# Performance work log

Hardware: AMD Instinct MI355X
Metric: run time of the kernel (lower is better)

## Reference

```python
import jax, jax.numpy as jnp
import numpy as np

N = 50000      # total nodes (batched protein graphs)
D = 256        # prot_hidden_dim
E = 800000     # edges per relation type
R = 5          # edge types: SEQ, STR_KNN, STR_DIS, SURF, LRR_REGION
LN_EPS = 1e-5
SIGMOID_TEMP = 2.0
WEIGHT_SCALE = 2.0
MIN_W, MAX_W = 0.05, 2.0


def setup_inputs() -> dict:
    key = jax.random.key(0)
    ks = jax.random.split(key, 8)
    x = jax.random.normal(ks[0], (N, D), dtype=jnp.float32)
    src = jax.random.randint(ks[1], (R, E), 0, N)
    dst = jax.random.randint(ks[2], (R, E), 0, N)
    # relation-attention MLP params: Linear(D, D//4) -> LayerNorm(D//4) -> ReLU -> Linear(D//4, 1)
    H = D // 4
    W1 = jax.random.normal(ks[3], (D, H), dtype=jnp.float32) / np.float32(np.sqrt(D))
    b1 = jnp.zeros((H,), jnp.float32)
    gamma = jnp.ones((H,), jnp.float32)
    beta = jnp.zeros((H,), jnp.float32)
    W2 = jax.random.normal(ks[4], (H, 1), dtype=jnp.float32) / np.float32(np.sqrt(H))
    b2 = jnp.zeros((1,), jnp.float32)
    attn_bias = jnp.array([-4.0, -4.0, -4.0, -4.0, -2.772], jnp.float32)
    return {"x": x, "src": src, "dst": dst, "W1": W1, "b1": b1,
            "gamma": gamma, "beta": beta, "W2": W2, "b2": b2,
            "attn_bias": attn_bias}


def _mean_aggregate(x, s, d):
    # DGL update_all(copy_u('h','m'), mean('m','h')): scatter-mean of src feats onto dst.
    sums = jax.ops.segment_sum(x[s], d, num_segments=N)                      # [N, D]
    cnt = jax.ops.segment_sum(jnp.ones((E,), x.dtype), d, num_segments=N)    # [N]
    # zero in-degree nodes get 0 (DGL mean semantics)
    return jnp.where(cnt[:, None] > 0, sums / jnp.maximum(cnt, 1.0)[:, None], 0.0)


def reference(x, src, dst, W1, b1, gamma, beta, W2, b2, attn_bias):
    # per-relation mean aggregation (loop over fixed small R, not a data dim)
    agg = jnp.stack([_mean_aggregate(x, src[r], dst[r]) for r in range(R)])  # [R, N, D]
    g = agg.mean(axis=1)                                                     # [R, D]
    # relation-attention MLP (dropout = identity in eval)
    h = g @ W1 + b1                                                          # [R, D//4]
    mu = h.mean(axis=-1, keepdims=True)
    var = ((h - mu) ** 2).mean(axis=-1, keepdims=True)
    h = (h - mu) * jax.lax.rsqrt(var + LN_EPS) * gamma + beta
    h = jax.nn.relu(h)
    scores = (h @ W2 + b2)[:, 0] + attn_bias                                 # [R]
    w = jax.nn.sigmoid(scores / SIGMOID_TEMP) * WEIGHT_SCALE
    w = jnp.clip(w, MIN_W, MAX_W)
    # fused = sum_r w[r] * agg[r]
    return jnp.einsum('r,rnd->nd', w, agg)
```

## Files before the change

### kernel.cpp

```cpp
#include <hip/hip_runtime.h>

#define NN 50000
#define DD 256
#define EE 800000
#define RR 5
#define HH 64
#define RN (RR * NN)

#define F_OFF  (RN)
#define F_CUR  (2 * RN)
#define F_C    (3 * RN)
#define F_G    (4 * RN)
#define F_W    (4 * RN + 1280)
#define F_CTR  (4 * RN + 1288)
#define F_ESRC (4 * RN + 1296)
#define F_XH   (F_ESRC + RR * EE)
#define BYTES_BF16 ((size_t)(F_XH + NN * DD / 2) * 4)
#define BYTES_F32  ((size_t)(F_ESRC + RR * EE) * 4)

#define C2_OFF  (RN)
#define C2_CUR  (2 * RN)
#define C2_G    (3 * RN)
#define C2_W    (3 * RN + 1280)
#define C2_CTR  (3 * RN + 1288)
#define C2_ESRC (3 * RN + 1296)
#define BYTES_CSR2 ((size_t)(C2_ESRC + RR * EE) * 4)

__device__ inline unsigned short bf16rn(float f) {
    unsigned u = __float_as_uint(f);
    unsigned r = u + 0x7FFFu + ((u >> 16) & 1u);
    return (unsigned short)(r >> 16);
}

__global__ __launch_bounds__(256) void deg_kernel(const int* __restrict__ dst,
                                                  int* __restrict__ cnt) {
    int i = blockIdx.x * 256 + threadIdx.x;
    if (i < RR * EE) {
        int r = i / EE;
        atomicAdd(&cnt[r * NN + dst[i]], 1);
    }
}

__global__ __launch_bounds__(256) void off_kernel(int* cnt, int* __restrict__ off,
                                                  int* __restrict__ cur,
                                                  int* __restrict__ ctr, float* invc) {
    int i = blockIdx.x * 256 + threadIdx.x;
    if (i < RN) {
        int cv = cnt[i];
        int o = atomicAdd(ctr, cv);
        off[i] = o;
        cur[i] = o;
        invc[i] = (cv > 0) ? (1.0f / (float)cv) : 0.0f;
    }
}

template <bool WITH_C>
__global__ __launch_bounds__(256) void fill_kernel(const int* __restrict__ src,
                                                   const int* __restrict__ dst,
                                                   int* __restrict__ cur,
                                                   int* __restrict__ esrc,
                                                   const float* __restrict__ invc,
                                                   float* __restrict__ c) {
    int i = blockIdx.x * 256 + threadIdx.x;
    if (i < RR * EE) {
        int r = i / EE;
        int d = dst[i];
        int s = src[i];
        int slot = atomicAdd(&cur[r * NN + d], 1);
        esrc[slot] = s;
        if constexpr (WITH_C) {
            unsafeAtomicAdd(&c[r * NN + s], invc[r * NN + d]);
        }
    }
}

__global__ __launch_bounds__(256) void gmat_kernel(const float* __restrict__ x,
                                                   const float* __restrict__ c,
                                                   float* __restrict__ g) {
    const int wave = threadIdx.x >> 6;
    const int lane = threadIdx.x & 63;
    const int gw = blockIdx.x * 4 + wave;
    const int nw = gridDim.x * 4;
    float4 a0 = {0, 0, 0, 0}, a1 = {0, 0, 0, 0}, a2 = {0, 0, 0, 0},
           a3 = {0, 0, 0, 0}, a4 = {0, 0, 0, 0};
    for (int s = gw; s < NN; s += nw) {
        float4 v = ((const float4*)(x + (size_t)s * DD))[lane];
        float c0 = c[0 * NN + s], c1 = c[1 * NN + s], c2 = c[2 * NN + s],
              c3 = c[3 * NN + s], c4 = c[4 * NN + s];
        a0.x += c0 * v.x; a0.y += c0 * v.y; a0.z += c0 * v.z; a0.w += c0 * v.w;
        a1.x += c1 * v.x; a1.y += c1 * v.y; a1.z += c1 * v.z; a1.w += c1 * v.w;
        a2.x += c2 * v.x; a2.y += c2 * v.y; a2.z += c2 * v.z; a2.w += c2 * v.w;
        a3.x += c3 * v.x; a3.y += c3 * v.y; a3.z += c3 * v.z; a3.w += c3 * v.w;
        a4.x += c4 * v.x; a4.y += c4 * v.y; a4.z += c4 * v.z; a4.w += c4 * v.w;
    }
    float4 acc[5] = {a0, a1, a2, a3, a4};
    #pragma unroll
    for (int r = 0; r < RR; ++r) {
        float* gr = g + r * DD + lane * 4;
        unsafeAtomicAdd(gr + 0, acc[r].x);
        unsafeAtomicAdd(gr + 1, acc[r].y);
        unsafeAtomicAdd(gr + 2, acc[r].z);
        unsafeAtomicAdd(gr + 3, acc[r].w);
    }
}

__global__ __launch_bounds__(256) void g_kernel(const float* __restrict__ x,
                                                const int* __restrict__ src,
                                                const int* __restrict__ dst,
                                                const float* __restrict__ invc,
                                                float* __restrict__ g) {
    const int r = blockIdx.y;
    const int wave = threadIdx.x >> 6;
    const int lane = threadIdx.x & 63;
    const int gw = blockIdx.x * 4 + wave;
    const int nw = gridDim.x * 4;
    const int* __restrict__ srcR = src + r * EE;
    const int* __restrict__ dstR = dst + r * EE;
    const float* __restrict__ invcR = invc + r * NN;
    float4 acc = {0, 0, 0, 0};
    for (int e = gw; e < EE; e += nw) {
        int eu = __builtin_amdgcn_readfirstlane(e);
        int s = srcR[eu];
        int dn = dstR[eu];
        float ic = invcR[dn];
        float4 v = ((const float4*)(x + (size_t)s * DD))[lane];
        acc.x += v.x * ic; acc.y += v.y * ic; acc.z += v.z * ic; acc.w += v.w * ic;
    }
    float* gr = g + r * DD + lane * 4;
    unsafeAtomicAdd(gr + 0, acc.x);
    unsafeAtomicAdd(gr + 1, acc.y);
    unsafeAtomicAdd(gr + 2, acc.z);
    unsafeAtomicAdd(gr + 3, acc.w);
}

__global__ __launch_bounds__(64) void mlp_kernel(const float* __restrict__ gsum,
                                                 const float* __restrict__ W1,
                                                 const float* __restrict__ b1,
                                                 const float* __restrict__ gamma,
                                                 const float* __restrict__ beta,
                                                 const float* __restrict__ W2,
                                                 const float* __restrict__ b2,
                                                 const float* __restrict__ attn_bias,
                                                 float* __restrict__ w) {
    const int t = threadIdx.x;
    __shared__ float gs[DD];
    const float invN = 1.0f / (float)NN;
    for (int r = 0; r < RR; ++r) {
        for (int d = t; d < DD; d += 64) gs[d] = gsum[r * DD + d] * invN;
        __syncthreads();
        float h = b1[t];
        for (int d = 0; d < DD; ++d) h += gs[d] * W1[d * HH + t];
        float mu = h;
        #pragma unroll
        for (int o = 32; o; o >>= 1) mu += __shfl_xor(mu, o, 64);
        mu *= (1.0f / 64.0f);
        float cc = h - mu;
        float var = cc * cc;
        #pragma unroll
        for (int o = 32; o; o >>= 1) var += __shfl_xor(var, o, 64);
        var *= (1.0f / 64.0f);
        float hn = cc * rsqrtf(var + 1e-5f) * gamma[t] + beta[t];
        hn = fmaxf(hn, 0.0f);
        float sc = hn * W2[t];
        #pragma unroll
        for (int o = 32; o; o >>= 1) sc += __shfl_xor(sc, o, 64);
        if (t == 0) {
            float s = sc + b2[0] + attn_bias[r];
            float ww = 2.0f / (1.0f + expf(-s * 0.5f));
            ww = fminf(fmaxf(ww, 0.05f), 2.0f);
            w[r] = ww;
        }
        __syncthreads();
    }
}

__global__ __launch_bounds__(256) void xcvt_kernel(const float* __restrict__ x,
                                                   ushort4* __restrict__ xh) {
    int i = blockIdx.x * 256 + threadIdx.x;
    if (i < NN * DD / 4) {
        float4 v = ((const float4*)x)[i];
        ushort4 q;
        q.x = bf16rn(v.x); q.y = bf16rn(v.y); q.z = bf16rn(v.z); q.w = bf16rn(v.w);
        xh[i] = q;
    }
}

template <bool BF16>
__device__ inline float4 loadrow(const float* __restrict__ x,
                                 const ushort4* __restrict__ xh, int s, int lane) {
    if constexpr (BF16) {
        ushort4 q = xh[(size_t)s * (DD / 4) + lane];
        float4 v;
        v.x = __uint_as_float((unsigned)q.x << 16);
        v.y = __uint_as_float((unsigned)q.y << 16);
        v.z = __uint_as_float((unsigned)q.z << 16);
        v.w = __uint_as_float((unsigned)q.w << 16);
        return v;
    } else {
        return ((const float4*)(x + (size_t)s * DD))[lane];
    }
}

template <bool BF16>
__global__ __launch_bounds__(256) void out_pull_kernel(const float* __restrict__ x,
                                                       const ushort4* __restrict__ xh,
                                                       const int* __restrict__ esrc,
                                                       const int* __restrict__ off,
                                                       const int* __restrict__ endv,
                                                       const float* __restrict__ invc,
                                                       const float* __restrict__ w,
                                                       float* __restrict__ out) {
    const int node = blockIdx.x * 4 + (threadIdx.x >> 6);
    if (node >= NN) return;
    const int lane = threadIdx.x & 63;

    float4 acc = {0, 0, 0, 0};
    #pragma unroll
    for (int r = 0; r < RR; ++r) {
        const int idx = r * NN + node;
        const int b = __builtin_amdgcn_readfirstlane(off[idx]);
        const int e_ = __builtin_amdgcn_readfirstlane(endv[idx]);
        const float coef = w[r] * invc[idx];
        float4 t = {0, 0, 0, 0};
        int e = b;
        for (; e + 4 <= e_; e += 4) {
            int s0 = __builtin_amdgcn_readfirstlane(esrc[e + 0]);
            int s1 = __builtin_amdgcn_readfirstlane(esrc[e + 1]);
            int s2 = __builtin_amdgcn_readfirstlane(esrc[e + 2]);
            int s3 = __builtin_amdgcn_readfirstlane(esrc[e + 3]);
            float4 v0 = loadrow<BF16>(x, xh, s0, lane);
            float4 v1 = loadrow<BF16>(x, xh, s1, lane);
            float4 v2 = loadrow<BF16>(x, xh, s2, lane);
            float4 v3 = loadrow<BF16>(x, xh, s3, lane);
            t.x += (v0.x + v1.x) + (v2.x + v3.x);
            t.y += (v0.y + v1.y) + (v2.y + v3.y);
            t.z += (v0.z + v1.z) + (v2.z + v3.z);
            t.w += (v0.w + v1.w) + (v2.w + v3.w);
        }
        for (; e < e_; ++e) {
            int s = __builtin_amdgcn_readfirstlane(esrc[e]);
            float4 v = loadrow<BF16>(x, xh, s, lane);
            t.x += v.x; t.y += v.y; t.z += v.z; t.w += v.w;
        }
        acc.x += coef * t.x; acc.y += coef * t.y;
        acc.z += coef * t.z; acc.w += coef * t.w;
    }
    ((float4*)(out + (size_t)node * DD))[lane] = acc;
}

__global__ __launch_bounds__(256) void invcnt_kernel(float* __restrict__ c) {
    int i = blockIdx.x * 256 + threadIdx.x;
    if (i < RN) {
        int v = ((const int*)c)[i];
        c[i] = (v > 0) ? (1.0f / (float)v) : 0.0f;
    }
}

__global__ __launch_bounds__(256) void out_scatter_kernel(const float* __restrict__ x,
                                                          const int* __restrict__ src,
                                                          const int* __restrict__ dst,
                                                          const float* __restrict__ invc,
                                                          const float* __restrict__ w,
                                                          float* __restrict__ out) {
    const int r = blockIdx.y;
    const float wr = w[r];
    const int wave = threadIdx.x >> 6;
    const int lane = threadIdx.x & 63;
    const int gw = blockIdx.x * 4 + wave;
    const int nw = gridDim.x * 4;
    const int* __restrict__ srcR = src + r * EE;
    const int* __restrict__ dstR = dst + r * EE;
    const float* __restrict__ invcR = invc + r * NN;
    for (int e = gw; e < EE; e += nw) {
        int eu = __builtin_amdgcn_readfirstlane(e);
        int s = srcR[eu];
        int dn = dstR[eu];
        float coef = wr * invcR[dn];
        float4 v = ((const float4*)(x + (size_t)s * DD))[lane];
        float* o = out + (size_t)dn * DD + lane * 4;
        unsafeAtomicAdd(o + 0, v.x * coef);
        unsafeAtomicAdd(o + 1, v.y * coef);
        unsafeAtomicAdd(o + 2, v.z * coef);
        unsafeAtomicAdd(o + 3, v.w * coef);
    }
}

extern "C" void kernel_launch(void* const* d_in, const int* in_sizes, int n_in,
                              void* d_out, int out_size, void* d_ws, size_t ws_size,
                              hipStream_t stream) {
    const float* x = (const float*)d_in[0];
    const int* src = (const int*)d_in[1];
    const int* dst = (const int*)d_in[2];
    const float* W1 = (const float*)d_in[3];
    const float* b1 = (const float*)d_in[4];
    const float* gamma = (const float*)d_in[5];
    const float* beta = (const float*)d_in[6];
    const float* W2 = (const float*)d_in[7];
    const float* b2 = (const float*)d_in[8];
    const float* attn_bias = (const float*)d_in[9];
    float* out = (float*)d_out;
    float* ws = (float*)d_ws;

    const int EDGE_GRID = (RR * EE + 255) / 256;
    const int RN_GRID = (RN + 255) / 256;

    if (ws_size >= BYTES_F32) {
        const bool bf16 = (ws_size >= BYTES_BF16);
        int* cnt = (int*)ws;
        float* invc = ws;
        int* off = (int*)ws + F_OFF;
        int* cur = (int*)ws + F_CUR;
        float* c = ws + F_C;
        float* g = ws + F_G;
        float* w = ws + F_W;
        int* ctr = (int*)ws + F_CTR;
        int* esrc = (int*)ws + F_ESRC;
        ushort4* xh = (ushort4*)((int*)ws + F_XH);

        hipMemsetAsync(cnt, 0, (size_t)RN * 4, stream);
        hipMemsetAsync(c, 0, (size_t)(RN + 1296) * 4, stream);

        if (bf16)
            xcvt_kernel<<<(NN * DD / 4 + 255) / 256, 256, 0, stream>>>(x, xh);
        deg_kernel<<<EDGE_GRID, 256, 0, stream>>>(dst, cnt);
        off_kernel<<<RN_GRID, 256, 0, stream>>>(cnt, off, cur, ctr, invc);
        fill_kernel<true><<<EDGE_GRID, 256, 0, stream>>>(src, dst, cur, esrc, invc, c);
        gmat_kernel<<<128, 256, 0, stream>>>(x, c, g);
        mlp_kernel<<<1, 64, 0, stream>>>(g, W1, b1, gamma, beta, W2, b2, attn_bias, w);
        if (bf16)
            out_pull_kernel<true><<<(NN + 3) / 4, 256, 0, stream>>>(x, xh, esrc, off,
                                                                    cur, invc, w, out);
        else
            out_pull_kernel<false><<<(NN + 3) / 4, 256, 0, stream>>>(x, xh, esrc, off,
                                                                     cur, invc, w, out);
    } else if (ws_size >= BYTES_CSR2) {
        int* cnt = (int*)ws;
        float* invc = ws;
        int* off = (int*)ws + C2_OFF;
        int* cur = (int*)ws + C2_CUR;
        float* g = ws + C2_G;
        float* w = ws + C2_W;
        int* ctr = (int*)ws + C2_CTR;
        int* esrc = (int*)ws + C2_ESRC;

        hipMemsetAsync(cnt, 0, (size_t)RN * 4, stream);
        hipMemsetAsync(g, 0, (size_t)1296 * 4, stream);

        deg_kernel<<<EDGE_GRID, 256, 0, stream>>>(dst, cnt);
        off_kernel<<<RN_GRID, 256, 0, stream>>>(cnt, off, cur, ctr, invc);
        fill_kernel<false><<<EDGE_GRID, 256, 0, stream>>>(src, dst, cur, esrc, invc,
                                                          nullptr);
        g_kernel<<<dim3(512, RR), 256, 0, stream>>>(x, src, dst, invc, g);
        mlp_kernel<<<1, 64, 0, stream>>>(g, W1, b1, gamma, beta, W2, b2, attn_bias, w);
        out_pull_kernel<false><<<(NN + 3) / 4, 256, 0, stream>>>(x, nullptr, esrc, off,
                                                                 cur, invc, w, out);
    } else {
        float* cnt = ws;
        float* g = ws + RN;
        float* w = ws + RN + RR * DD;
        hipMemsetAsync(ws, 0, (size_t)(RN + RR * DD + RR) * 4, stream);
        hipMemsetAsync(d_out, 0, (size_t)NN * DD * 4, stream);
        deg_kernel<<<EDGE_GRID, 256, 0, stream>>>(dst, (int*)cnt);
        invcnt_kernel<<<RN_GRID, 256, 0, stream>>>(cnt);
        g_kernel<<<dim3(512, RR), 256, 0, stream>>>(x, src, dst, cnt, g);
        mlp_kernel<<<1, 64, 0, stream>>>(g, W1, b1, gamma, beta, W2, b2, attn_bias, w);
        out_scatter_kernel<<<dim3(512, RR), 256, 0, stream>>>(x, src, dst, cnt, w, out);
    }
}
```

Before: 1.137 ms.

## Build node-major CSR with 16-bit sources and scan-based offsets for pull aggregation

Adds a new path that computes CSR offsets with a block-sum plus scan, ordered node-major with relations interleaved. Source indices are stored as 16-bit values, and the edge fill is split into two destination-range passes. A new pull kernel walks all five relations of a node contiguously, unrolling bf16 row gathers by four. The aim is to improve locality of the scatter and gather and to cut index bandwidth, at the cost of extra kernel launches and a second pass over the edge list.

```diff
diff --git a/kernel.cpp b/kernel.cpp
--- a/kernel.cpp
+++ b/kernel.cpp
@@ -6,6 +6,18 @@
 #define RR 5
 #define HH 64
 #define RN (RR * NN)
+#define NBLK ((NN + 255) / 256)
+
+#define P_OFF   (RN)
+#define P_CUR   (2 * RN)
+#define P_C     (3 * RN)
+#define P_G     (4 * RN)
+#define P_W     (4 * RN + 1280)
+#define P_BSUM  (4 * RN + 1288)
+#define P_BBASE (4 * RN + 1544)
+#define P_ESRC  (4 * RN + 1800)
+#define P_XH    (P_ESRC + RR * EE / 2)
+#define BYTES_NEW ((size_t)(P_XH + NN * DD / 2) * 4)
 
 #define F_OFF  (RN)
 #define F_CUR  (2 * RN)
@@ -41,34 +53,87 @@
     }
 }
 
-__global__ __launch_bounds__(256) void off_kernel(int* cnt, int* __restrict__ off,
-                                                  int* __restrict__ cur,
-                                                  int* __restrict__ ctr, float* invc) {
-    int i = blockIdx.x * 256 + threadIdx.x;
-    if (i < RN) {
-        int cv = cnt[i];
-        int o = atomicAdd(ctr, cv);
-        off[i] = o;
-        cur[i] = o;
-        invc[i] = (cv > 0) ? (1.0f / (float)cv) : 0.0f;
-    }
-}
-
-template <bool WITH_C>
-__global__ __launch_bounds__(256) void fill_kernel(const int* __restrict__ src,
-                                                   const int* __restrict__ dst,
-                                                   int* __restrict__ cur,
-                                                   int* __restrict__ esrc,
-                                                   const float* __restrict__ invc,
-                                                   float* __restrict__ c) {
+__global__ __launch_bounds__(256) void bsum_kernel(const int* __restrict__ cnt,
+                                                   int* __restrict__ bsum) {
+    __shared__ int sh[256];
+    const int t = threadIdx.x;
+    const int d = blockIdx.x * 256 + t;
+    int tot = 0;
+    if (d < NN) {
+        #pragma unroll
+        for (int r = 0; r < RR; ++r) tot += cnt[r * NN + d];
+    }
+    sh[t] = tot;
+    __syncthreads();
+    for (int o = 128; o; o >>= 1) {
+        if (t < o) sh[t] += sh[t + o];
+        __syncthreads();
+    }
+    if (t == 0) bsum[blockIdx.x] = sh[0];
+}
+
+__global__ void bscan_kernel(const int* __restrict__ bsum, int* __restrict__ bbase) {
+    if (threadIdx.x == 0) {
+        int acc = 0;
+        for (int b = 0; b < NBLK; ++b) {
+            bbase[b] = acc;
+            acc += bsum[b];
+        }
+    }
+}
+
+__global__ __launch_bounds__(256) void off2_kernel(int* __restrict__ cnt_invc,
+                                                   const int* __restrict__ bbase,
+                                                   int* __restrict__ off,
+                                                   int* __restrict__ cur) {
+    __shared__ int sh[256];
+    const int t = threadIdx.x;
+    const int d = blockIdx.x * 256 + t;
+    int cc[RR];
+    int tot = 0;
+    if (d < NN) {
+        #pragma unroll
+        for (int r = 0; r < RR; ++r) {
+            cc[r] = cnt_invc[r * NN + d];
+            tot += cc[r];
+        }
+    }
+    sh[t] = tot;
+    __syncthreads();
+    for (int o = 1; o < 256; o <<= 1) {
+        int v = (t >= o) ? sh[t - o] : 0;
+        __syncthreads();
+        sh[t] += v;
+        __syncthreads();
+    }
+    if (d < NN) {
+        int base = bbase[blockIdx.x] + sh[t] - tot;
+        float* invc = (float*)cnt_invc;
+        #pragma unroll
+        for (int r = 0; r < RR; ++r) {
+            off[d * RR + r] = base;
+            cur[d * RR + r] = base;
+            base += cc[r];
+            invc[r * NN + d] = (cc[r] > 0) ? (1.0f / (float)cc[r]) : 0.0f;
+        }
+    }
+}
+
+__global__ __launch_bounds__(256) void fill2_kernel(const int* __restrict__ src,
+                                                    const int* __restrict__ dst,
+                                                    int* __restrict__ cur,
+                                                    unsigned short* __restrict__ esrc,
+                                                    const float* __restrict__ invc,
+                                                    float* __restrict__ c,
+                                                    int dlo, int dhi) {
     int i = blockIdx.x * 256 + threadIdx.x;
     if (i < RR * EE) {
-        int r = i / EE;
         int d = dst[i];
-        int s = src[i];
-        int slot = atomicAdd(&cur[r * NN + d], 1);
-        esrc[slot] = s;
-        if constexpr (WITH_C) {
+        if (d >= dlo && d < dhi) {
+            int r = i / EE;
+            int s = src[i];
+            int slot = atomicAdd(&cur[d * RR + r], 1);
+            esrc[slot] = (unsigned short)s;
             unsafeAtomicAdd(&c[r * NN + s], invc[r * NN + d]);
         }
     }
@@ -102,35 +167,6 @@
         unsafeAtomicAdd(gr + 2, acc[r].z);
         unsafeAtomicAdd(gr + 3, acc[r].w);
     }
-}
-
-__global__ __launch_bounds__(256) void g_kernel(const float* __restrict__ x,
-                                                const int* __restrict__ src,
-                                                const int* __restrict__ dst,
-                                                const float* __restrict__ invc,
-                                                float* __restrict__ g) {
-    const int r = blockIdx.y;
-    const int wave = threadIdx.x >> 6;
-    const int lane = threadIdx.x & 63;
-    const int gw = blockIdx.x * 4 + wave;
-    const int nw = gridDim.x * 4;
-    const int* __restrict__ srcR = src + r * EE;
-    const int* __restrict__ dstR = dst + r * EE;
-    const float* __restrict__ invcR = invc + r * NN;
-    float4 acc = {0, 0, 0, 0};
-    for (int e = gw; e < EE; e += nw) {
-        int eu = __builtin_amdgcn_readfirstlane(e);
-        int s = srcR[eu];
-        int dn = dstR[eu];
-        float ic = invcR[dn];
-        float4 v = ((const float4*)(x + (size_t)s * DD))[lane];
-        acc.x += v.x * ic; acc.y += v.y * ic; acc.z += v.z * ic; acc.w += v.w * ic;
-    }
-    float* gr = g + r * DD + lane * 4;
-    unsafeAtomicAdd(gr + 0, acc.x);
-    unsafeAtomicAdd(gr + 1, acc.y);
-    unsafeAtomicAdd(gr + 2, acc.z);
-    unsafeAtomicAdd(gr + 3, acc.w);
 }
 
 __global__ __launch_bounds__(64) void mlp_kernel(const float* __restrict__ gsum,
@@ -185,17 +221,127 @@
     }
 }
 
+__device__ inline float4 bf16row(const ushort4* __restrict__ xh, int s, int lane) {
+    ushort4 q = xh[(size_t)s * (DD / 4) + lane];
+    float4 v;
+    v.x = __uint_as_float((unsigned)q.x << 16);
+    v.y = __uint_as_float((unsigned)q.y << 16);
+    v.z = __uint_as_float((unsigned)q.z << 16);
+    v.w = __uint_as_float((unsigned)q.w << 16);
+    return v;
+}
+
+__global__ __launch_bounds__(256) void out_pull2_kernel(const ushort4* __restrict__ xh,
+                                                        const unsigned short* __restrict__ esrc,
+                                                        const int* __restrict__ off,
+                                                        const int* __restrict__ endv,
+                                                        const float* __restrict__ invc,
+                                                        const float* __restrict__ w,
+                                                        float* __restrict__ out) {
+    const int node = blockIdx.x * 4 + (threadIdx.x >> 6);
+    if (node >= NN) return;
+    const int lane = threadIdx.x & 63;
+
+    float4 acc = {0, 0, 0, 0};
+    #pragma unroll
+    for (int r = 0; r < RR; ++r) {
+        const int b = __builtin_amdgcn_readfirstlane(off[node * RR + r]);
+        const int e_ = __builtin_amdgcn_readfirstlane(endv[node * RR + r]);
+        const float coef = w[r] * invc[r * NN + node];
+        float4 t = {0, 0, 0, 0};
+        int e = b;
+        for (; e + 4 <= e_; e += 4) {
+            int s0 = __builtin_amdgcn_readfirstlane((int)esrc[e + 0]);
+            int s1 = __builtin_amdgcn_readfirstlane((int)esrc[e + 1]);
+            int s2 = __builtin_amdgcn_readfirstlane((int)esrc[e + 2]);
+            int s3 = __builtin_amdgcn_readfirstlane((int)esrc[e + 3]);
+            float4 v0 = bf16row(xh, s0, lane);
+            float4 v1 = bf16row(xh, s1, lane);
+            float4 v2 = bf16row(xh, s2, lane);
+            float4 v3 = bf16row(xh, s3, lane);
+            t.x += (v0.x + v1.x) + (v2.x + v3.x);
+            t.y += (v0.y + v1.y) + (v2.y + v3.y);
+            t.z += (v0.z + v1.z) + (v2.z + v3.z);
+            t.w += (v0.w + v1.w) + (v2.w + v3.w);
+        }
+        for (; e < e_; ++e) {
+            int s = __builtin_amdgcn_readfirstlane((int)esrc[e]);
+            float4 v = bf16row(xh, s, lane);
+            t.x += v.x; t.y += v.y; t.z += v.z; t.w += v.w;
+        }
+        acc.x += coef * t.x; acc.y += coef * t.y;
+        acc.z += coef * t.z; acc.w += coef * t.w;
+    }
+    ((float4*)(out + (size_t)node * DD))[lane] = acc;
+}
+
+__global__ __launch_bounds__(256) void off_kernel(int* cnt, int* __restrict__ off,
+                                                  int* __restrict__ cur,
+                                                  int* __restrict__ ctr, float* invc) {
+    int i = blockIdx.x * 256 + threadIdx.x;
+    if (i < RN) {
+        int cv = cnt[i];
+        int o = atomicAdd(ctr, cv);
+        off[i] = o;
+        cur[i] = o;
+        invc[i] = (cv > 0) ? (1.0f / (float)cv) : 0.0f;
+    }
+}
+
+template <bool WITH_C>
+__global__ __launch_bounds__(256) void fill_kernel(const int* __restrict__ src,
+                                                   const int* __restrict__ dst,
+                                                   int* __restrict__ cur,
+                                                   int* __restrict__ esrc,
+                                                   const float* __restrict__ invc,
+                                                   float* __restrict__ c) {
+    int i = blockIdx.x * 256 + threadIdx.x;
+    if (i < RR * EE) {
+        int r = i / EE;
+        int d = dst[i];
+        int s = src[i];
+        int slot = atomicAdd(&cur[r * NN + d], 1);
+        esrc[slot] = s;
+        if constexpr (WITH_C) {
+            unsafeAtomicAdd(&c[r * NN + s], invc[r * NN + d]);
+        }
+    }
+}
+
+__global__ __launch_bounds__(256) void g_kernel(const float* __restrict__ x,
+                                                const int* __restrict__ src,
+                                                const int* __restrict__ dst,
+                                                const float* __restrict__ invc,
+                                                float* __restrict__ g) {
+    const int r = blockIdx.y;
+    const int wave = threadIdx.x >> 6;
+    const int lane = threadIdx.x & 63;
+    const int gw = blockIdx.x * 4 + wave;
+    const int nw = gridDim.x * 4;
+    const int* __restrict__ srcR = src + r * EE;
+    const int* __restrict__ dstR = dst + r * EE;
+    const float* __restrict__ invcR = invc + r * NN;
+    float4 acc = {0, 0, 0, 0};
+    for (int e = gw; e < EE; e += nw) {
+        int eu = __builtin_amdgcn_readfirstlane(e);
+        int s = srcR[eu];
+        int dn = dstR[eu];
+        float ic = invcR[dn];
+        float4 v = ((const float4*)(x + (size_t)s * DD))[lane];
+        acc.x += v.x * ic; acc.y += v.y * ic; acc.z += v.z * ic; acc.w += v.w * ic;
+    }
+    float* gr = g + r * DD + lane * 4;
+    unsafeAtomicAdd(gr + 0, acc.x);
+    unsafeAtomicAdd(gr + 1, acc.y);
+    unsafeAtomicAdd(gr + 2, acc.z);
+    unsafeAtomicAdd(gr + 3, acc.w);
+}
+
 template <bool BF16>
 __device__ inline float4 loadrow(const float* __restrict__ x,
                                  const ushort4* __restrict__ xh, int s, int lane) {
     if constexpr (BF16) {
-        ushort4 q = xh[(size_t)s * (DD / 4) + lane];
-        float4 v;
-        v.x = __uint_as_float((unsigned)q.x << 16);
-        v.y = __uint_as_float((unsigned)q.y << 16);
-        v.z = __uint_as_float((unsigned)q.z << 16);
-        v.w = __uint_as_float((unsigned)q.w << 16);
-        return v;
+        return bf16row(xh, s, lane);
     } else {
         return ((const float4*)(x + (size_t)s * DD))[lane];
     }
@@ -304,7 +450,36 @@
     const int EDGE_GRID = (RR * EE + 255) / 256;
     const int RN_GRID = (RN + 255) / 256;
 
-    if (ws_size >= BYTES_F32) {
+    if (ws_size >= BYTES_NEW) {
+        int* cnt = (int*)ws;
+        float* invc = ws;
+        int* off = (int*)ws + P_OFF;
+        int* cur = (int*)ws + P_CUR;
+        float* c = ws + P_C;
+        float* g = ws + P_G;
+        float* w = ws + P_W;
+        int* bsum = (int*)ws + P_BSUM;
+        int* bbase = (int*)ws + P_BBASE;
+        unsigned short* esrc = (unsigned short*)((int*)ws + P_ESRC);
+        ushort4* xh = (ushort4*)((int*)ws + P_XH);
+
+        hipMemsetAsync(cnt, 0, (size_t)RN * 4, stream);
+        hipMemsetAsync(c, 0, (size_t)(RN + 1288) * 4, stream);
+
+        xcvt_kernel<<<(NN * DD / 4 + 255) / 256, 256, 0, stream>>>(x, xh);
+        deg_kernel<<<EDGE_GRID, 256, 0, stream>>>(dst, cnt);
+        bsum_kernel<<<NBLK, 256, 0, stream>>>(cnt, bsum);
+        bscan_kernel<<<1, 64, 0, stream>>>(bsum, bbase);
+        off2_kernel<<<NBLK, 256, 0, stream>>>(cnt, bbase, off, cur);
+        fill2_kernel<<<EDGE_GRID, 256, 0, stream>>>(src, dst, cur, esrc, invc, c,
+                                                    0, NN / 2);
+        fill2_kernel<<<EDGE_GRID, 256, 0, stream>>>(src, dst, cur, esrc, invc, c,
+                                                    NN / 2, NN);
+        gmat_kernel<<<128, 256, 0, stream>>>(x, c, g);
+        mlp_kernel<<<1, 64, 0, stream>>>(g, W1, b1, gamma, beta, W2, b2, attn_bias, w);
+        out_pull2_kernel<<<(NN + 3) / 4, 256, 0, stream>>>(xh, esrc, off, cur, invc,
+                                                           w, out);
+    } else if (ws_size >= BYTES_F32) {
         const bool bf16 = (ws_size >= BYTES_BF16);
         int* cnt = (int*)ws;
         float* invc = ws;
```

Result: faster. 1.091 ms (-4.1%).
